# Kernel optimization log

Hardware: AMD Instinct MI355X
Metric: run time of the kernel (lower is better)

## Reference

```python
import jax, jax.numpy as jnp
import numpy as np

QMAX = 127.0

def fake_quant(x):
    # per-tensor symmetric int8 fake quantize-dequantize (QAT)
    s = jnp.maximum(jnp.max(jnp.abs(x)) / QMAX, 1e-8)
    q = jnp.clip(jnp.round(x / s), -QMAX, QMAX) * s
    return x + jax.lax.stop_gradient(q - x)  # STE

def qlinear(x, w, b):
    # x already fake-quantized by caller (input_quantizer); weights fake-quantized here
    return jnp.einsum('btc,oc->bto', x, fake_quant(w)) + b

def layer_norm(x, g, b, eps=1e-5):
    m = jnp.mean(x, axis=-1, keepdims=True)
    v = jnp.var(x, axis=-1, keepdims=True)
    return (x - m) * jax.lax.rsqrt(v + eps) * g + b

def setup_inputs() -> dict:
    key = jax.random.key(0)
    ks = jax.random.split(key, 8)
    B, T, C, I = 8, 512, 1024, 4096
    sd = 0.02
    return {
        'hidden_states': jax.random.normal(ks[0], (B, T, C), jnp.float32),
        'attention_mask': jnp.ones((B, T), jnp.float32),
        'ln1_g': jnp.ones((C,), jnp.float32), 'ln1_b': jnp.zeros((C,), jnp.float32),
        'ln2_g': jnp.ones((C,), jnp.float32), 'ln2_b': jnp.zeros((C,), jnp.float32),
        'w_qkv': sd * jax.random.normal(ks[1], (3 * C, C), jnp.float32),
        'b_qkv': jnp.zeros((3 * C,), jnp.float32),
        'w_out': sd * jax.random.normal(ks[2], (C, C), jnp.float32),
        'b_out': jnp.zeros((C,), jnp.float32),
        'w1': sd * jax.random.normal(ks[3], (I, C), jnp.float32),
        'b1': jnp.zeros((I,), jnp.float32),
        'w2': sd * jax.random.normal(ks[4], (C, I), jnp.float32),
        'b2': jnp.zeros((C,), jnp.float32),
    }

def reference(hidden_states, attention_mask, ln1_g, ln1_b, ln2_g, ln2_b,
              w_qkv, b_qkv, w_out, b_out, w1, b1, w2, b2):
    B, T, C = hidden_states.shape
    H = 16
    Dh = C // H
    scale = Dh ** -0.5

    # --- attention branch (pre-norm) ---
    x = layer_norm(hidden_states, ln1_g, ln1_b)
    qkv = qlinear(fake_quant(x), w_qkv, b_qkv)            # [B,T,3C]
    qkv = qkv.reshape(B, T, 3, H, Dh).transpose(2, 0, 3, 1, 4)
    q, k, v = qkv[0], qkv[1], qkv[2]                       # [B,H,T,Dh]
    scores = jnp.einsum('bhqd,bhkd->bhqk', q, k) * scale
    ext = (1.0 - attention_mask)[:, None, None, :] * -10000.0
    scores = scores + ext
    attn = jax.nn.softmax(scores, axis=-1)
    out = jnp.einsum('bhqk,bhkd->bhqd', attn, v)
    out = out.transpose(0, 2, 1, 3).reshape(B, T, C)
    attn_out = qlinear(fake_quant(out), w_out, b_out)
    h = hidden_states + attn_out

    # --- MLP branch (pre-norm) ---
    x = layer_norm(h, ln2_g, ln2_b)
    x = qlinear(fake_quant(x), w1, b1)
    x = jax.nn.gelu(x, approximate=False)
    x = qlinear(fake_quant(x), w2, b2)
    return h + x
```

## Files before the change

kernel.cpp:

```cpp
#include <hip/hip_runtime.h>

typedef __attribute__((ext_vector_type(8))) short bf16x8;
typedef __attribute__((ext_vector_type(4))) float f32x4;
typedef __attribute__((ext_vector_type(4))) int i32x4;
typedef unsigned short u16;
typedef unsigned int u32;

#define B_ 8
#define T_ 512
#define C_ 1024
#define I_ 4096
#define H_ 16
#define Dh_ 64
#define BT (B_*T_)
#define NH (B_*H_)

__device__ __forceinline__ float bf2f(u16 u) {
  return __uint_as_float(((u32)u) << 16);
}
__device__ __forceinline__ u16 f2bf(float f) {
  u32 u = __float_as_uint(f);
  u32 r = u + 0x7FFFu + ((u >> 16) & 1u);
  return (u16)(r >> 16);
}
__device__ __forceinline__ float wredMax(float v) {
#pragma unroll
  for (int o = 32; o; o >>= 1) v = fmaxf(v, __shfl_xor(v, o));
  return v;
}
__device__ __forceinline__ float wredSum(float v) {
#pragma unroll
  for (int o = 32; o; o >>= 1) v += __shfl_xor(v, o);
  return v;
}
__device__ __forceinline__ void slotAtomicMax(u32* arr, int bid, float bm) {
  u32 b = __float_as_uint(bm);
  volatile u32* p = arr + ((bid & 63) << 4);
  if (b > *p) atomicMax((u32*)p, b);
}
__device__ __forceinline__ float slotMax(const u32* __restrict__ arr) {
  float m = 0.f;
#pragma unroll
  for (int i = 0; i < 64; ++i) m = fmaxf(m, __uint_as_float(arr[i << 4]));
  return m;
}
__device__ __forceinline__ void gload16(const void* g, void* l) {
  __builtin_amdgcn_global_load_lds((const __attribute__((address_space(1))) void*)g,
                                   (__attribute__((address_space(3))) void*)l, 16, 0, 0);
}
__device__ __forceinline__ int qi(float v, float inv) {
  return (int)fminf(fmaxf(rintf(v * inv), -127.f), 127.f);
}
__device__ __forceinline__ float gelu1(float v) {
  float x2 = v * v;
  float e = __expf(v * fmaf(-0.0713548755f, x2, -1.5957691216f));
  return v * __builtin_amdgcn_rcpf(1.0f + e);
}

__global__ void k_init(u32* s) {
  int i = blockIdx.x * 256 + threadIdx.x;
  if (i < 8192) s[i] = 0u;
}

__global__ __launch_bounds__(256) void k_absmax4(
    const float* __restrict__ p0, int n0,
    const float* __restrict__ p1, int n1,
    const float* __restrict__ p2, int n2,
    const float* __restrict__ p3, int n3,
    u32* __restrict__ sc) {
  int stride = gridDim.x * blockDim.x;
  int gid = blockIdx.x * blockDim.x + threadIdx.x;
  float m0 = 0.f, m1 = 0.f, m2 = 0.f, m3 = 0.f;
  for (int i = gid; i < n0; i += stride) {
    float4 v = ((const float4*)p0)[i];
    m0 = fmaxf(m0, fmaxf(fmaxf(fabsf(v.x), fabsf(v.y)), fmaxf(fabsf(v.z), fabsf(v.w))));
  }
  for (int i = gid; i < n1; i += stride) {
    float4 v = ((const float4*)p1)[i];
    m1 = fmaxf(m1, fmaxf(fmaxf(fabsf(v.x), fabsf(v.y)), fmaxf(fabsf(v.z), fabsf(v.w))));
  }
  for (int i = gid; i < n2; i += stride) {
    float4 v = ((const float4*)p2)[i];
    m2 = fmaxf(m2, fmaxf(fmaxf(fabsf(v.x), fabsf(v.y)), fmaxf(fabsf(v.z), fabsf(v.w))));
  }
  for (int i = gid; i < n3; i += stride) {
    float4 v = ((const float4*)p3)[i];
    m3 = fmaxf(m3, fmaxf(fmaxf(fabsf(v.x), fabsf(v.y)), fmaxf(fabsf(v.z), fabsf(v.w))));
  }
  m0 = wredMax(m0); m1 = wredMax(m1); m2 = wredMax(m2); m3 = wredMax(m3);
  __shared__ float red[4][4];
  int wid = threadIdx.x >> 6, lane = threadIdx.x & 63;
  if (lane == 0) { red[wid][0] = m0; red[wid][1] = m1; red[wid][2] = m2; red[wid][3] = m3; }
  __syncthreads();
  if (threadIdx.x < 4) {
    int j = threadIdx.x;
    float bm = fmaxf(fmaxf(red[0][j], red[1][j]), fmaxf(red[2][j], red[3][j]));
    slotAtomicMax(sc + j * 1024, blockIdx.x, bm);
  }
}

__global__ __launch_bounds__(256) void k_quant4(
    const float* __restrict__ p0, signed char* __restrict__ q0, int n0,
    const float* __restrict__ p1, signed char* __restrict__ q1, int n1,
    const float* __restrict__ p2, signed char* __restrict__ q2, int n2,
    const float* __restrict__ p3, signed char* __restrict__ q3, int n3,
    const u32* __restrict__ sc) {
  int stride = gridDim.x * blockDim.x;
  int gid = blockIdx.x * blockDim.x + threadIdx.x;
#define QLOOP(p, q, n, slot)                                                        \
  {                                                                                 \
    float s = fmaxf(slotMax(sc + slot * 1024) * (1.0f / 127.0f), 1e-8f);            \
    float inv = 1.0f / s;                                                           \
    for (int i = gid; i < n; i += stride) {                                         \
      float4 v = ((const float4*)p)[i];                                             \
      u32 pk = (u32)(qi(v.x, inv) & 255) | ((u32)(qi(v.y, inv) & 255) << 8) |       \
               ((u32)(qi(v.z, inv) & 255) << 16) | ((u32)(qi(v.w, inv) & 255) << 24); \
      ((u32*)q)[i] = pk;                                                            \
    }                                                                               \
  }
  QLOOP(p0, q0, n0, 0)
  QLOOP(p1, q1, n1, 1)
  QLOOP(p2, q2, n2, 2)
  QLOOP(p3, q3, n3, 3)
#undef QLOOP
}

__global__ __launch_bounds__(256) void k_quant_b8(const u16* __restrict__ x, signed char* __restrict__ q,
                                                  int n8, const u32* __restrict__ arr) {
  float s = fmaxf(slotMax(arr) * (1.0f / 127.0f), 1e-8f);
  float inv = 1.0f / s;
  int stride = gridDim.x * blockDim.x;
  for (int i = blockIdx.x * blockDim.x + threadIdx.x; i < n8; i += stride) {
    uint4 d = ((const uint4*)x)[i];
    u16* e = (u16*)&d;
    uint2 o;
    o.x = (u32)(qi(bf2f(e[0]), inv) & 255) | ((u32)(qi(bf2f(e[1]), inv) & 255) << 8) |
          ((u32)(qi(bf2f(e[2]), inv) & 255) << 16) | ((u32)(qi(bf2f(e[3]), inv) & 255) << 24);
    o.y = (u32)(qi(bf2f(e[4]), inv) & 255) | ((u32)(qi(bf2f(e[5]), inv) & 255) << 8) |
          ((u32)(qi(bf2f(e[6]), inv) & 255) << 16) | ((u32)(qi(bf2f(e[7]), inv) & 255) << 24);
    ((uint2*)q)[i] = o;
  }
}

__global__ __launch_bounds__(256) void k_ln(const float* __restrict__ x, const float* __restrict__ g,
                                            const float* __restrict__ b, u16* __restrict__ y,
                                            u32* __restrict__ arr) {
  int row = blockIdx.x;
  int t = threadIdx.x;
  float4 v = ((const float4*)(x + (long)row * C_))[t];
  float s1 = v.x + v.y + v.z + v.w;
  float s2 = v.x * v.x + v.y * v.y + v.z * v.z + v.w * v.w;
  s1 = wredSum(s1);
  s2 = wredSum(s2);
  __shared__ float red[8];
  int wid = t >> 6, lane = t & 63;
  if (lane == 0) { red[wid] = s1; red[4 + wid] = s2; }
  __syncthreads();
  s1 = red[0] + red[1] + red[2] + red[3];
  s2 = red[4] + red[5] + red[6] + red[7];
  float mean = s1 * (1.0f / C_);
  float var = s2 * (1.0f / C_) - mean * mean;
  float inv = rsqrtf(var + 1e-5f);
  float4 gv = ((const float4*)g)[t];
  float4 bv = ((const float4*)b)[t];
  float4 o;
  o.x = (v.x - mean) * inv * gv.x + bv.x;
  o.y = (v.y - mean) * inv * gv.y + bv.y;
  o.z = (v.z - mean) * inv * gv.z + bv.z;
  o.w = (v.w - mean) * inv * gv.w + bv.w;
  ushort4 ob;
  ob.x = f2bf(o.x); ob.y = f2bf(o.y); ob.z = f2bf(o.z); ob.w = f2bf(o.w);
  ((ushort4*)(y + (long)row * C_))[t] = ob;
  float m = fmaxf(fmaxf(fabsf(o.x), fabsf(o.y)), fmaxf(fabsf(o.z), fabsf(o.w)));
  m = wredMax(m);
  __syncthreads();
  if (lane == 0) red[wid] = m;
  __syncthreads();
  if (t == 0) {
    float bm = fmaxf(fmaxf(red[0], red[1]), fmaxf(red[2], red[3]));
    slotAtomicMax(arr, row, bm);
  }
}

__global__ __launch_bounds__(256, 1) void k_attn(
    const u16* __restrict__ qkv, const float* __restrict__ mask,
    u16* __restrict__ O, u32* __restrict__ amax) {
  __shared__ u16 Ke[512 * 64];
  __shared__ u16 Vt[64 * 512];
  __shared__ u16 Pl[4 * 64 * 40];
  __shared__ float extl[512];
  __shared__ float redm[4];
  const int tid = threadIdx.x;
  const int w = tid >> 6, l = tid & 63;
  const int head = blockIdx.x;
  const int chunk = blockIdx.y;
  const int b = head >> 4, h = head & 15;
  const long rowbase = (long)(b * 512) * (3 * C_);

  {
    const u16* Kg = qkv + rowbase + C_ + h * 64;
    int lr8 = l >> 3;
    int ls = (l & 7) ^ lr8;
    const long koff = (long)lr8 * (3 * C_) + ls * 8;
#pragma unroll
    for (int i = 0; i < 16; ++i) {
      int r0 = w * 128 + i * 8;
      gload16(Kg + (long)r0 * (3 * C_) + koff, &Ke[r0 * 64]);
    }
  }
  {
    const u16* Vg = qkv + rowbase + 2 * C_ + h * 64;
    int kvl = tid & 31;
    int d0 = (tid >> 5) * 8;
#pragma unroll 4
    for (int i = 0; i < 16; ++i) {
      int kv = i * 32 + kvl;
      uint4 t4 = *(const uint4*)(Vg + (long)kv * (3 * C_) + d0);
      u16* tv = (u16*)&t4;
      int slot = kv >> 3, within = kv & 7;
#pragma unroll
      for (int j = 0; j < 8; ++j) {
        int d = d0 + j;
        Vt[d * 512 + ((slot ^ (d & 7)) << 3) + within] = tv[j];
      }
    }
  }
  {
    const float* mb = mask + b * 512;
    extl[tid] = (1.0f - mb[tid]) * -10000.0f;
    extl[tid + 256] = (1.0f - mb[tid + 256]) * -10000.0f;
  }
  const int qbase = chunk * 256 + w * 64;
  bf16x8 qf[4][2];
  {
    const u16* Qg = qkv + rowbase + h * 64;
#pragma unroll
    for (int qt = 0; qt < 4; ++qt)
#pragma unroll
      for (int dc = 0; dc < 2; ++dc)
        qf[qt][dc] = *(const bf16x8*)(Qg + (long)(qbase + qt * 16 + (l & 15)) * (3 * C_) + dc * 32 + (l >> 4) * 8);
  }
  __syncthreads();

  f32x4 oacc[4][4];
  float mrun[4], lrun[4];
#pragma unroll
  for (int qt = 0; qt < 4; ++qt) { mrun[qt] = -3.0e38f; lrun[qt] = 0.f; }
#pragma unroll
  for (int dt = 0; dt < 4; ++dt)
#pragma unroll
    for (int qt = 0; qt < 4; ++qt) oacc[dt][qt] = (f32x4){0.f, 0.f, 0.f, 0.f};

  u16* Pw = &Pl[w * 64 * 40];

  for (int ks = 0; ks < 16; ++ks) {
    bf16x8 kf[2][2];
#pragma unroll
    for (int kvt = 0; kvt < 2; ++kvt) {
      int kv = ks * 32 + kvt * 16 + (l & 15);
#pragma unroll
      for (int dc = 0; dc < 2; ++dc) {
        int phys = (dc * 4 + (l >> 4)) ^ (kv & 7);
        kf[kvt][dc] = *(const bf16x8*)&Ke[kv * 64 + phys * 8];
      }
    }
    f32x4 sacc[2][4];
#pragma unroll
    for (int kvt = 0; kvt < 2; ++kvt)
#pragma unroll
      for (int qt = 0; qt < 4; ++qt) {
        f32x4 a = (f32x4){0.f, 0.f, 0.f, 0.f};
        a = __builtin_amdgcn_mfma_f32_16x16x32_bf16(kf[kvt][0], qf[qt][0], a, 0, 0, 0);
        a = __builtin_amdgcn_mfma_f32_16x16x32_bf16(kf[kvt][1], qf[qt][1], a, 0, 0, 0);
        sacc[kvt][qt] = a;
      }
#pragma unroll
    for (int kvt = 0; kvt < 2; ++kvt) {
      f32x4 ev = *(const f32x4*)&extl[ks * 32 + kvt * 16 + (l >> 4) * 4];
#pragma unroll
      for (int qt = 0; qt < 4; ++qt)
#pragma unroll
        for (int r = 0; r < 4; ++r)
          sacc[kvt][qt][r] = fmaf(sacc[kvt][qt][r], 0.125f, ev[r]);
    }
#pragma unroll
    for (int qt = 0; qt < 4; ++qt) {
      float pm = sacc[0][qt][0];
#pragma unroll
      for (int r = 1; r < 4; ++r) pm = fmaxf(pm, sacc[0][qt][r]);
#pragma unroll
      for (int r = 0; r < 4; ++r) pm = fmaxf(pm, sacc[1][qt][r]);
      pm = fmaxf(pm, __shfl_xor(pm, 16));
      pm = fmaxf(pm, __shfl_xor(pm, 32));
      float mnew = fmaxf(mrun[qt], pm);
      float f = __expf(mrun[qt] - mnew);
      mrun[qt] = mnew;
      float lsum = 0.f;
#pragma unroll
      for (int kvt = 0; kvt < 2; ++kvt)
#pragma unroll
        for (int r = 0; r < 4; ++r) {
          float p = __expf(sacc[kvt][qt][r] - mnew);
          sacc[kvt][qt][r] = p;
          lsum += p;
        }
      lsum += __shfl_xor(lsum, 16);
      lsum += __shfl_xor(lsum, 32);
      lrun[qt] = lrun[qt] * f + lsum;
#pragma unroll
      for (int dt = 0; dt < 4; ++dt)
#pragma unroll
        for (int r = 0; r < 4; ++r) oacc[dt][qt][r] *= f;
#pragma unroll
      for (int kvt = 0; kvt < 2; ++kvt) {
        u32 p01 = (u32)f2bf(sacc[kvt][qt][0]) | ((u32)f2bf(sacc[kvt][qt][1]) << 16);
        u32 p23 = (u32)f2bf(sacc[kvt][qt][2]) | ((u32)f2bf(sacc[kvt][qt][3]) << 16);
        u16* pr = Pw + (qt * 16 + (l & 15)) * 40 + kvt * 16 + (l >> 4) * 4;
        *(u32*)pr = p01;
        *(u32*)(pr + 2) = p23;
      }
    }
    bf16x8 vf[4], pf[4];
#pragma unroll
    for (int dt = 0; dt < 4; ++dt) {
      int d = dt * 16 + (l & 15);
      int phys = (ks * 4 + (l >> 4)) ^ (d & 7);
      vf[dt] = *(const bf16x8*)&Vt[d * 512 + phys * 8];
    }
#pragma unroll
    for (int qt = 0; qt < 4; ++qt)
      pf[qt] = *(const bf16x8*)(Pw + (qt * 16 + (l & 15)) * 40 + (l >> 4) * 8);
#pragma unroll
    for (int dt = 0; dt < 4; ++dt)
#pragma unroll
      for (int qt = 0; qt < 4; ++qt)
        oacc[dt][qt] = __builtin_amdgcn_mfma_f32_16x16x32_bf16(vf[dt], pf[qt], oacc[dt][qt], 0, 0, 0);
  }

  float lmax = 0.f;
  u16* Ob = O + (long)(b * 512 + qbase) * C_ + h * 64;
#pragma unroll
  for (int qt = 0; qt < 4; ++qt) {
    float inv = 1.0f / lrun[qt];
    long qoff = (long)(qt * 16 + (l & 15)) * C_;
#pragma unroll
    for (int dt = 0; dt < 4; ++dt) {
      int d = dt * 16 + (l >> 4) * 4;
      float v0 = oacc[dt][qt][0] * inv;
      float v1 = oacc[dt][qt][1] * inv;
      float v2 = oacc[dt][qt][2] * inv;
      float v3 = oacc[dt][qt][3] * inv;
      lmax = fmaxf(fmaxf(lmax, fmaxf(fabsf(v0), fabsf(v1))), fmaxf(fabsf(v2), fabsf(v3)));
      u32 a01 = (u32)f2bf(v0) | ((u32)f2bf(v1) << 16);
      u32 a23 = (u32)f2bf(v2) | ((u32)f2bf(v3) << 16);
      *(u32*)(Ob + qoff + d) = a01;
      *(u32*)(Ob + qoff + d + 2) = a23;
    }
  }
  lmax = wredMax(lmax);
  if (l == 0) redm[w] = lmax;
  __syncthreads();
  if (tid == 0)
    slotAtomicMax(amax, blockIdx.x * 2 + blockIdx.y,
                  fmaxf(fmaxf(redm[0], redm[1]), fmaxf(redm[2], redm[3])));
}

template <int BM, int BN, int EPI, bool SWZ>
__global__ __launch_bounds__(256) void k_gemmq(
    const signed char* __restrict__ A, int lda,
    const signed char* __restrict__ Bm, int ldb,
    const float* __restrict__ bias,
    void* __restrict__ Cp, int ldc,
    int M, int N, int K,
    const float* __restrict__ resid,
    u32* __restrict__ amaxOut,
    const u32* __restrict__ amaxA, const u32* __restrict__ amaxB) {
  constexpr int BK = 128;
  constexpr int MF = (BM / 2) / 16;
  constexpr int NF = (BN / 2) / 16;
  constexpr int NLD = BM / 32 + BN / 32;
  __shared__ __align__(16) signed char As[2][BM * BK];
  __shared__ __align__(16) signed char Bs[2][BN * BK];
  const int tid = threadIdx.x;
  const int wid = tid >> 6, lane = tid & 63;
  const int wr = wid >> 1, wc = wid & 1;

  float sa = fmaxf(slotMax(amaxA) * (1.0f / 127.0f), 1e-8f);
  float sb = fmaxf(slotMax(amaxB) * (1.0f / 127.0f), 1e-8f);
  const float sAB = sa * sb;

  int bx = blockIdx.x, by = blockIdx.y;
  if (SWZ) {
    int gx = gridDim.x;
    int nwg = gx * gridDim.y;
    int bid = by * gx + bx;
    int cpx = nwg >> 3;
    int swz = (bid & 7) * cpx + (bid >> 3);
    bx = swz % gx;
    by = swz / gx;
  }

  const signed char* Ab = A + (long)by * BM * lda;
  const signed char* Bb = Bm + (long)bx * BN * ldb;

  i32x4 acc[MF][NF];
#pragma unroll
  for (int m = 0; m < MF; m++)
#pragma unroll
    for (int n = 0; n < NF; n++) acc[m][n] = (i32x4){0, 0, 0, 0};

  const int lr = lane & 15;
  const int l8 = lane >> 3;
  const int s8 = (lane & 7) ^ l8;
  const long aoff = (long)l8 * lda + s8 * 16;
  const long boff = (long)l8 * ldb + s8 * 16;

  auto stageAB = [&](int buf, int k0) {
#pragma unroll
    for (int i = 0; i < BM / 32; ++i) {
      int R0 = wid * (BM / 4) + i * 8;
      gload16(Ab + (long)R0 * lda + k0 + aoff, &As[buf][R0 * BK]);
    }
#pragma unroll
    for (int i = 0; i < BN / 32; ++i) {
      int R0 = wid * (BN / 4) + i * 8;
      gload16(Bb + (long)R0 * ldb + k0 + boff, &Bs[buf][R0 * BK]);
    }
  };

  auto waitCounted = [&]() {
    if constexpr (NLD == 8) {
      asm volatile("s_waitcnt vmcnt(8)" ::: "memory");
    } else if constexpr (NLD == 6) {
      asm volatile("s_waitcnt vmcnt(6)" ::: "memory");
    } else {
      asm volatile("s_waitcnt vmcnt(4)" ::: "memory");
    }
  };

  auto computeK = [&](int buf) {
#pragma unroll
    for (int kk = 0; kk < 2; ++kk) {
      const int sl = (kk << 2) + (lane >> 4);
      const int sf = (sl ^ (lr & 7)) << 4;
      i32x4 af[MF], bfr[NF];
#pragma unroll
      for (int m = 0; m < MF; m++)
        af[m] = *(const i32x4*)&As[buf][(wr * (BM / 2) + m * 16 + lr) * BK + sf];
#pragma unroll
      for (int n = 0; n < NF; n++)
        bfr[n] = *(const i32x4*)&Bs[buf][(wc * (BN / 2) + n * 16 + lr) * BK + sf];
      __builtin_amdgcn_s_setprio(1);
#pragma unroll
      for (int m = 0; m < MF; m++)
#pragma unroll
        for (int n = 0; n < NF; n++)
          acc[m][n] = __builtin_amdgcn_mfma_i32_16x16x64_i8(af[m], bfr[n], acc[m][n], 0, 0, 0);
      __builtin_amdgcn_s_setprio(0);
    }
  };

  const int nt = K / BK;
  stageAB(0, 0);
  int cur = 0;
  for (int t = 0; t < nt; ++t) {
    if (t + 1 < nt) {
      stageAB(cur ^ 1, (t + 1) * BK);
      waitCounted();
    } else {
      asm volatile("s_waitcnt vmcnt(0)" ::: "memory");
    }
    __builtin_amdgcn_s_barrier();
    computeK(cur);
    if (t + 1 < nt)
      __builtin_amdgcn_s_barrier();
    cur ^= 1;
  }

  const int rowBase = by * BM + wr * (BM / 2);
  const int colBase = bx * BN + wc * (BN / 2);
  float lmax = 0.f;
#pragma unroll
  for (int m = 0; m < MF; m++) {
    int row0 = rowBase + m * 16 + (lane >> 4) * 4;
#pragma unroll
    for (int n = 0; n < NF; n++) {
      int col = colBase + n * 16 + lr;
      float bs = bias[col];
#pragma unroll
      for (int j = 0; j < 4; j++) {
        int row = row0 + j;
        long idx = (long)row * ldc + col;
        float v = (float)acc[m][n][j] * sAB;
        if (EPI == 0) {
          ((u16*)Cp)[idx] = f2bf(v + bs);
        } else if (EPI == 1) {
          ((float*)Cp)[idx] = v + bs + resid[idx];
        } else if (EPI == 2) {
          v = gelu1(v + bs);
          lmax = fmaxf(fmaxf(lmax, v), 0.0f - v);
          ((u16*)Cp)[idx] = f2bf(v);
        } else if (EPI == 3) {
          ((float*)Cp)[idx] = v + bs + resid[idx];
        }
      }
    }
  }
  if (EPI == 2) {
    __shared__ float redm[4];
    float wm = wredMax(lmax);
    if (lane == 0) redm[wid] = wm;
    __syncthreads();
    if (tid == 0) {
      float bm = fmaxf(fmaxf(redm[0], redm[1]), fmaxf(redm[2], redm[3]));
      slotAtomicMax(amaxOut, blockIdx.y * gridDim.x + blockIdx.x, bm);
    }
  }
}

__global__ __launch_bounds__(512, 1) void k_gemmq8(
    const signed char* __restrict__ A, int lda,
    const signed char* __restrict__ Bm, int ldb,
    const float* __restrict__ bias,
    u16* __restrict__ Cp, int ldc,
    int K,
    u32* __restrict__ amaxOut,
    const u32* __restrict__ amaxA, const u32* __restrict__ amaxB) {
  __shared__ __align__(16) signed char As[2][256 * 128];
  __shared__ __align__(16) signed char Bs[2][256 * 128];
  const int tid = threadIdx.x;
  const int wid = tid >> 6, lane = tid & 63;
  const int wr = wid >> 2, wc = wid & 3;
  const int lr = lane & 15;

  float sa = fmaxf(slotMax(amaxA) * (1.0f / 127.0f), 1e-8f);
  float sb = fmaxf(slotMax(amaxB) * (1.0f / 127.0f), 1e-8f);
  const float sAB = sa * sb;

  int bx = blockIdx.x, by = blockIdx.y;
  {
    int bid = by * 16 + bx;
    int swz = (bid & 7) * 32 + (bid >> 3);
    bx = swz & 15;
    by = swz >> 4;
  }
  const signed char* Ab = A + (long)by * 256 * lda;
  const signed char* Bb = Bm + (long)bx * 256 * ldb;

  i32x4 acc[8][4];
#pragma unroll
  for (int m = 0; m < 8; m++)
#pragma unroll
    for (int n = 0; n < 4; n++) acc[m][n] = (i32x4){0, 0, 0, 0};

  const int l8 = lane >> 3;
  const int s8 = (lane & 7) ^ l8;
  const long aoff = (long)l8 * lda + s8 * 16;
  const long boff = (long)l8 * ldb + s8 * 16;

  auto stageHalf = [&](int buf, int kt, int h) {
    int k0 = kt * 128;
    if (h < 2) {
      int R0 = h * 128 + wid * 16;
      gload16(Ab + (long)R0 * lda + k0 + aoff, &As[buf][R0 * 128]);
      gload16(Ab + (long)(R0 + 8) * lda + k0 + aoff, &As[buf][(R0 + 8) * 128]);
    } else {
      int R0 = (h - 2) * 128 + wid * 16;
      gload16(Bb + (long)R0 * ldb + k0 + boff, &Bs[buf][R0 * 128]);
      gload16(Bb + (long)(R0 + 8) * ldb + k0 + boff, &Bs[buf][(R0 + 8) * 128]);
    }
  };

  const int nt = K / 128;
#define PHASE(BUF, MH, KS, STAGESTMT)                                              \
  {                                                                                \
    const int slotl = (KS) * 4 + (lane >> 4);                                      \
    i32x4 af[4], bfr[4];                                                           \
    _Pragma("unroll") for (int i = 0; i < 4; ++i) {                                \
      int row = wr * 128 + ((MH) * 4 + i) * 16 + lr;                               \
      af[i] = *(const i32x4*)&As[BUF][row * 128 + ((slotl ^ (row & 7)) << 4)];     \
    }                                                                              \
    _Pragma("unroll") for (int n = 0; n < 4; ++n) {                                \
      int row = wc * 64 + n * 16 + lr;                                             \
      bfr[n] = *(const i32x4*)&Bs[BUF][row * 128 + ((slotl ^ (row & 7)) << 4)];    \
    }                                                                              \
    STAGESTMT;                                                                     \
    __builtin_amdgcn_s_barrier();                                                  \
    __builtin_amdgcn_s_setprio(1);                                                 \
    _Pragma("unroll") for (int i = 0; i < 4; ++i)                                  \
      _Pragma("unroll") for (int n = 0; n < 4; ++n)                                \
        acc[(MH) * 4 + i][n] =                                                     \
            __builtin_amdgcn_mfma_i32_16x16x64_i8(af[i], bfr[n], acc[(MH) * 4 + i][n], 0, 0, 0); \
    __builtin_amdgcn_s_setprio(0);                                                 \
    __builtin_amdgcn_s_barrier();                                                  \
  }

  stageHalf(0, 0, 0);
  stageHalf(0, 0, 2);
  stageHalf(0, 0, 3);
  stageHalf(0, 0, 1);

  int cur = 0;
  for (int t = 0; t < nt; ++t) {
    const bool stg = (t + 1 < nt);
    const int nb = cur ^ 1;
    const int tn = t + 1;
    asm volatile("s_waitcnt vmcnt(2)" ::: "memory");
    __builtin_amdgcn_s_barrier();
    PHASE(cur, 0, 0, { if (stg) stageHalf(nb, tn, 0); })
    PHASE(cur, 0, 1, { if (stg) stageHalf(nb, tn, 2); })
    if (stg) {
      asm volatile("s_waitcnt vmcnt(4)" ::: "memory");
    } else {
      asm volatile("s_waitcnt vmcnt(0)" ::: "memory");
    }
    __builtin_amdgcn_s_barrier();
    PHASE(cur, 1, 0, { if (stg) stageHalf(nb, tn, 3); })
    PHASE(cur, 1, 1, { if (stg) stageHalf(nb, tn, 1); })
    cur = nb;
  }
#undef PHASE

  const int rowBase = by * 256 + wr * 128;
  const int colBase = bx * 256 + wc * 64;
  float lmax = 0.f;
#pragma unroll
  for (int m = 0; m < 8; m++) {
    int row0 = rowBase + m * 16 + (lane >> 4) * 4;
#pragma unroll
    for (int n = 0; n < 4; n++) {
      int col = colBase + n * 16 + lr;
      float bs = bias[col];
#pragma unroll
      for (int j = 0; j < 4; j++) {
        long idx = (long)(row0 + j) * ldc + col;
        float v = gelu1((float)acc[m][n][j] * sAB + bs);
        lmax = fmaxf(fmaxf(lmax, v), 0.0f - v);
        Cp[idx] = f2bf(v);
      }
    }
  }
  {
    __shared__ float redm[8];
    float wm = wredMax(lmax);
    if (lane == 0) redm[wid] = wm;
    __syncthreads();
    if (tid == 0) {
      float bm = redm[0];
#pragma unroll
      for (int i = 1; i < 8; ++i) bm = fmaxf(bm, redm[i]);
      slotAtomicMax(amaxOut, blockIdx.y * gridDim.x + blockIdx.x, bm);
    }
  }
}

extern "C" void kernel_launch(void* const* d_in, const int* in_sizes, int n_in,
                              void* d_out, int out_size, void* d_ws, size_t ws_size,
                              hipStream_t stream) {
  const float* hidden = (const float*)d_in[0];
  const float* mask = (const float*)d_in[1];
  const float* ln1g = (const float*)d_in[2];
  const float* ln1b = (const float*)d_in[3];
  const float* ln2g = (const float*)d_in[4];
  const float* ln2b = (const float*)d_in[5];
  const float* w_qkv = (const float*)d_in[6];
  const float* b_qkv = (const float*)d_in[7];
  const float* w_out = (const float*)d_in[8];
  const float* b_out = (const float*)d_in[9];
  const float* w1 = (const float*)d_in[10];
  const float* b1 = (const float*)d_in[11];
  const float* w2 = (const float*)d_in[12];
  const float* b2 = (const float*)d_in[13];

  char* ws = (char*)d_ws;
  u32* sc = (u32*)ws;
  const long MB = 1024 * 1024;
  signed char* wq_qkv = (signed char*)(ws + 1 * MB);
  signed char* wq_out = (signed char*)(ws + 4 * MB);
  signed char* wq_w1  = (signed char*)(ws + 6 * MB);
  signed char* wq_w2  = (signed char*)(ws + 10 * MB);
  signed char* xq     = (signed char*)(ws + 14 * MB);
  u16* x1             = (u16*)(ws + 18 * MB);
  signed char* Oq     = (signed char*)(ws + 26 * MB);
  u16* O              = (u16*)(ws + 30 * MB);
  u16* qkv            = (u16*)(ws + 38 * MB);
  float* hbuf         = (float*)(ws + 62 * MB);
  u16* y1             = (u16*)(ws + 78 * MB);
  signed char* y1q    = (signed char*)(ws + 110 * MB);

  k_init<<<32, 256, 0, stream>>>(sc);

  k_absmax4<<<512, 256, 0, stream>>>(
      w_qkv, 3 * C_ * C_ / 4, w_out, C_ * C_ / 4, w1, I_ * C_ / 4, w2, C_ * I_ / 4, sc);
  k_quant4<<<512, 256, 0, stream>>>(
      w_qkv, wq_qkv, 3 * C_ * C_ / 4, w_out, wq_out, C_ * C_ / 4,
      w1, wq_w1, I_ * C_ / 4, w2, wq_w2, C_ * I_ / 4, sc);

  k_ln<<<BT, 256, 0, stream>>>(hidden, ln1g, ln1b, x1, sc + 4 * 1024);
  k_quant_b8<<<512, 256, 0, stream>>>(x1, xq, BT * C_ / 8, sc + 4 * 1024);

  k_gemmq<128, 128, 0, true><<<dim3(24, 32), 256, 0, stream>>>(
      xq, C_, wq_qkv, C_, b_qkv, qkv, 3 * C_,
      BT, 3 * C_, C_, nullptr, nullptr, sc + 4 * 1024, sc + 0 * 1024);

  k_attn<<<dim3(NH, 2), 256, 0, stream>>>(qkv, mask, O, sc + 5 * 1024);
  k_quant_b8<<<512, 256, 0, stream>>>(O, Oq, BT * C_ / 8, sc + 5 * 1024);

  k_gemmq<64, 64, 1, true><<<dim3(16, 64), 256, 0, stream>>>(
      Oq, C_, wq_out, C_, b_out, hbuf, C_,
      BT, C_, C_, hidden, nullptr, sc + 5 * 1024, sc + 1 * 1024);

  k_ln<<<BT, 256, 0, stream>>>(hbuf, ln2g, ln2b, x1, sc + 6 * 1024);
  k_quant_b8<<<512, 256, 0, stream>>>(x1, xq, BT * C_ / 8, sc + 6 * 1024);

  k_gemmq8<<<dim3(16, 16), 512, 0, stream>>>(
      xq, C_, wq_w1, C_, b1, y1, I_, C_,
      sc + 7 * 1024, sc + 6 * 1024, sc + 2 * 1024);
  k_quant_b8<<<512, 256, 0, stream>>>(y1, y1q, BT * I_ / 8, sc + 7 * 1024);

  k_gemmq<64, 64, 3, true><<<dim3(16, 64), 256, 0, stream>>>(
      y1q, I_, wq_w2, I_, b2, d_out, C_,
      BT, C_, I_, hbuf, nullptr, sc + 7 * 1024, sc + 3 * 1024);
}
```

Baseline: 241.6 us.

## Merge weight prequant with first layernorm and store residual h in bf16

Fuses weight absmax with the first layernorm into one launch, and weight quantization with the activation quantization into a second launch. This removes two kernel launches and lets the independent work share the GPU. It also stores the intermediate residual h as bf16 instead of fp32, halving its write and its two reads (LN2 input and final residual). The cost is reduced precision in the residual path, which may move outputs away from the fp32 reference.

```diff
diff --git a/kernel.cpp b/kernel.cpp
--- a/kernel.cpp
+++ b/kernel.cpp
@@ -62,67 +62,127 @@
   if (i < 8192) s[i] = 0u;
 }
 
-__global__ __launch_bounds__(256) void k_absmax4(
+__global__ __launch_bounds__(256) void k_pre1(
     const float* __restrict__ p0, int n0,
     const float* __restrict__ p1, int n1,
     const float* __restrict__ p2, int n2,
     const float* __restrict__ p3, int n3,
-    u32* __restrict__ sc) {
-  int stride = gridDim.x * blockDim.x;
-  int gid = blockIdx.x * blockDim.x + threadIdx.x;
-  float m0 = 0.f, m1 = 0.f, m2 = 0.f, m3 = 0.f;
-  for (int i = gid; i < n0; i += stride) {
-    float4 v = ((const float4*)p0)[i];
-    m0 = fmaxf(m0, fmaxf(fmaxf(fabsf(v.x), fabsf(v.y)), fmaxf(fabsf(v.z), fabsf(v.w))));
-  }
-  for (int i = gid; i < n1; i += stride) {
-    float4 v = ((const float4*)p1)[i];
-    m1 = fmaxf(m1, fmaxf(fmaxf(fabsf(v.x), fabsf(v.y)), fmaxf(fabsf(v.z), fabsf(v.w))));
-  }
-  for (int i = gid; i < n2; i += stride) {
-    float4 v = ((const float4*)p2)[i];
-    m2 = fmaxf(m2, fmaxf(fmaxf(fabsf(v.x), fabsf(v.y)), fmaxf(fabsf(v.z), fabsf(v.w))));
-  }
-  for (int i = gid; i < n3; i += stride) {
-    float4 v = ((const float4*)p3)[i];
-    m3 = fmaxf(m3, fmaxf(fmaxf(fabsf(v.x), fabsf(v.y)), fmaxf(fabsf(v.z), fabsf(v.w))));
-  }
-  m0 = wredMax(m0); m1 = wredMax(m1); m2 = wredMax(m2); m3 = wredMax(m3);
-  __shared__ float red[4][4];
-  int wid = threadIdx.x >> 6, lane = threadIdx.x & 63;
-  if (lane == 0) { red[wid][0] = m0; red[wid][1] = m1; red[wid][2] = m2; red[wid][3] = m3; }
-  __syncthreads();
-  if (threadIdx.x < 4) {
-    int j = threadIdx.x;
-    float bm = fmaxf(fmaxf(red[0][j], red[1][j]), fmaxf(red[2][j], red[3][j]));
-    slotAtomicMax(sc + j * 1024, blockIdx.x, bm);
-  }
-}
-
-__global__ __launch_bounds__(256) void k_quant4(
+    u32* __restrict__ scw,
+    const float* __restrict__ x, const float* __restrict__ g,
+    const float* __restrict__ b, u16* __restrict__ y,
+    u32* __restrict__ arr) {
+  const int t = threadIdx.x;
+  if (blockIdx.x < 512) {
+    int stride = 512 * 256;
+    int gid = blockIdx.x * 256 + t;
+    float m0 = 0.f, m1 = 0.f, m2 = 0.f, m3 = 0.f;
+    for (int i = gid; i < n0; i += stride) {
+      float4 v = ((const float4*)p0)[i];
+      m0 = fmaxf(m0, fmaxf(fmaxf(fabsf(v.x), fabsf(v.y)), fmaxf(fabsf(v.z), fabsf(v.w))));
+    }
+    for (int i = gid; i < n1; i += stride) {
+      float4 v = ((const float4*)p1)[i];
+      m1 = fmaxf(m1, fmaxf(fmaxf(fabsf(v.x), fabsf(v.y)), fmaxf(fabsf(v.z), fabsf(v.w))));
+    }
+    for (int i = gid; i < n2; i += stride) {
+      float4 v = ((const float4*)p2)[i];
+      m2 = fmaxf(m2, fmaxf(fmaxf(fabsf(v.x), fabsf(v.y)), fmaxf(fabsf(v.z), fabsf(v.w))));
+    }
+    for (int i = gid; i < n3; i += stride) {
+      float4 v = ((const float4*)p3)[i];
+      m3 = fmaxf(m3, fmaxf(fmaxf(fabsf(v.x), fabsf(v.y)), fmaxf(fabsf(v.z), fabsf(v.w))));
+    }
+    m0 = wredMax(m0); m1 = wredMax(m1); m2 = wredMax(m2); m3 = wredMax(m3);
+    __shared__ float red4[4][4];
+    int wid = t >> 6, lane = t & 63;
+    if (lane == 0) { red4[wid][0] = m0; red4[wid][1] = m1; red4[wid][2] = m2; red4[wid][3] = m3; }
+    __syncthreads();
+    if (t < 4) {
+      int j = t;
+      float bm = fmaxf(fmaxf(red4[0][j], red4[1][j]), fmaxf(red4[2][j], red4[3][j]));
+      slotAtomicMax(scw + j * 1024, blockIdx.x, bm);
+    }
+  } else {
+    int row = blockIdx.x - 512;
+    float4 v = ((const float4*)(x + (long)row * C_))[t];
+    float s1 = v.x + v.y + v.z + v.w;
+    float s2 = v.x * v.x + v.y * v.y + v.z * v.z + v.w * v.w;
+    s1 = wredSum(s1);
+    s2 = wredSum(s2);
+    __shared__ float red[8];
+    int wid = t >> 6, lane = t & 63;
+    if (lane == 0) { red[wid] = s1; red[4 + wid] = s2; }
+    __syncthreads();
+    s1 = red[0] + red[1] + red[2] + red[3];
+    s2 = red[4] + red[5] + red[6] + red[7];
+    float mean = s1 * (1.0f / C_);
+    float var = s2 * (1.0f / C_) - mean * mean;
+    float inv = rsqrtf(var + 1e-5f);
+    float4 gv = ((const float4*)g)[t];
+    float4 bv = ((const float4*)b)[t];
+    float4 o;
+    o.x = (v.x - mean) * inv * gv.x + bv.x;
+    o.y = (v.y - mean) * inv * gv.y + bv.y;
+    o.z = (v.z - mean) * inv * gv.z + bv.z;
+    o.w = (v.w - mean) * inv * gv.w + bv.w;
+    ushort4 ob;
+    ob.x = f2bf(o.x); ob.y = f2bf(o.y); ob.z = f2bf(o.z); ob.w = f2bf(o.w);
+    ((ushort4*)(y + (long)row * C_))[t] = ob;
+    float m = fmaxf(fmaxf(fabsf(o.x), fabsf(o.y)), fmaxf(fabsf(o.z), fabsf(o.w)));
+    m = wredMax(m);
+    __syncthreads();
+    if (lane == 0) red[wid] = m;
+    __syncthreads();
+    if (t == 0) {
+      float bm = fmaxf(fmaxf(red[0], red[1]), fmaxf(red[2], red[3]));
+      slotAtomicMax(arr, row, bm);
+    }
+  }
+}
+
+__global__ __launch_bounds__(256) void k_pre2(
     const float* __restrict__ p0, signed char* __restrict__ q0, int n0,
     const float* __restrict__ p1, signed char* __restrict__ q1, int n1,
     const float* __restrict__ p2, signed char* __restrict__ q2, int n2,
     const float* __restrict__ p3, signed char* __restrict__ q3, int n3,
-    const u32* __restrict__ sc) {
-  int stride = gridDim.x * blockDim.x;
-  int gid = blockIdx.x * blockDim.x + threadIdx.x;
+    const u32* __restrict__ scw,
+    const u16* __restrict__ xb, signed char* __restrict__ xq, int n8,
+    const u32* __restrict__ arrX) {
+  const int t = threadIdx.x;
+  if (blockIdx.x < 512) {
+    int stride = 512 * 256;
+    int gid = blockIdx.x * 256 + t;
 #define QLOOP(p, q, n, slot)                                                        \
-  {                                                                                 \
-    float s = fmaxf(slotMax(sc + slot * 1024) * (1.0f / 127.0f), 1e-8f);            \
-    float inv = 1.0f / s;                                                           \
-    for (int i = gid; i < n; i += stride) {                                         \
-      float4 v = ((const float4*)p)[i];                                             \
-      u32 pk = (u32)(qi(v.x, inv) & 255) | ((u32)(qi(v.y, inv) & 255) << 8) |       \
-               ((u32)(qi(v.z, inv) & 255) << 16) | ((u32)(qi(v.w, inv) & 255) << 24); \
-      ((u32*)q)[i] = pk;                                                            \
-    }                                                                               \
-  }
-  QLOOP(p0, q0, n0, 0)
-  QLOOP(p1, q1, n1, 1)
-  QLOOP(p2, q2, n2, 2)
-  QLOOP(p3, q3, n3, 3)
+    {                                                                               \
+      float s = fmaxf(slotMax(scw + slot * 1024) * (1.0f / 127.0f), 1e-8f);         \
+      float inv = 1.0f / s;                                                         \
+      for (int i = gid; i < n; i += stride) {                                       \
+        float4 v = ((const float4*)p)[i];                                           \
+        u32 pk = (u32)(qi(v.x, inv) & 255) | ((u32)(qi(v.y, inv) & 255) << 8) |     \
+                 ((u32)(qi(v.z, inv) & 255) << 16) | ((u32)(qi(v.w, inv) & 255) << 24); \
+        ((u32*)q)[i] = pk;                                                          \
+      }                                                                             \
+    }
+    QLOOP(p0, q0, n0, 0)
+    QLOOP(p1, q1, n1, 1)
+    QLOOP(p2, q2, n2, 2)
+    QLOOP(p3, q3, n3, 3)
 #undef QLOOP
+  } else {
+    float s = fmaxf(slotMax(arrX) * (1.0f / 127.0f), 1e-8f);
+    float inv = 1.0f / s;
+    int stride = 512 * 256;
+    for (int i = (blockIdx.x - 512) * 256 + t; i < n8; i += stride) {
+      uint4 d = ((const uint4*)xb)[i];
+      u16* e = (u16*)&d;
+      uint2 o;
+      o.x = (u32)(qi(bf2f(e[0]), inv) & 255) | ((u32)(qi(bf2f(e[1]), inv) & 255) << 8) |
+            ((u32)(qi(bf2f(e[2]), inv) & 255) << 16) | ((u32)(qi(bf2f(e[3]), inv) & 255) << 24);
+      o.y = (u32)(qi(bf2f(e[4]), inv) & 255) | ((u32)(qi(bf2f(e[5]), inv) & 255) << 8) |
+            ((u32)(qi(bf2f(e[6]), inv) & 255) << 16) | ((u32)(qi(bf2f(e[7]), inv) & 255) << 24);
+      ((uint2*)xq)[i] = o;
+    }
+  }
 }
 
 __global__ __launch_bounds__(256) void k_quant_b8(const u16* __restrict__ x, signed char* __restrict__ q,
@@ -142,12 +202,14 @@
   }
 }
 
-__global__ __launch_bounds__(256) void k_ln(const float* __restrict__ x, const float* __restrict__ g,
-                                            const float* __restrict__ b, u16* __restrict__ y,
-                                            u32* __restrict__ arr) {
+__global__ __launch_bounds__(256) void k_lnb(const u16* __restrict__ x, const float* __restrict__ g,
+                                             const float* __restrict__ b, u16* __restrict__ y,
+                                             u32* __restrict__ arr) {
   int row = blockIdx.x;
   int t = threadIdx.x;
-  float4 v = ((const float4*)(x + (long)row * C_))[t];
+  ushort4 xb = ((const ushort4*)(x + (long)row * C_))[t];
+  float4 v;
+  v.x = bf2f(xb.x); v.y = bf2f(xb.y); v.z = bf2f(xb.z); v.w = bf2f(xb.w);
   float s1 = v.x + v.y + v.z + v.w;
   float s2 = v.x * v.x + v.y * v.y + v.z * v.z + v.w * v.w;
   s1 = wredSum(s1);
@@ -372,7 +434,7 @@
     const float* __restrict__ bias,
     void* __restrict__ Cp, int ldc,
     int M, int N, int K,
-    const float* __restrict__ resid,
+    const void* __restrict__ resid,
     u32* __restrict__ amaxOut,
     const u32* __restrict__ amaxA, const u32* __restrict__ amaxB) {
   constexpr int BK = 128;
@@ -495,13 +557,13 @@
         if (EPI == 0) {
           ((u16*)Cp)[idx] = f2bf(v + bs);
         } else if (EPI == 1) {
-          ((float*)Cp)[idx] = v + bs + resid[idx];
+          ((u16*)Cp)[idx] = f2bf(v + bs + ((const float*)resid)[idx]);
         } else if (EPI == 2) {
           v = gelu1(v + bs);
           lmax = fmaxf(fmaxf(lmax, v), 0.0f - v);
           ((u16*)Cp)[idx] = f2bf(v);
         } else if (EPI == 3) {
-          ((float*)Cp)[idx] = v + bs + resid[idx];
+          ((float*)Cp)[idx] = v + bs + bf2f(((const u16*)resid)[idx]);
         }
       }
     }
@@ -684,20 +746,20 @@
   signed char* Oq     = (signed char*)(ws + 26 * MB);
   u16* O              = (u16*)(ws + 30 * MB);
   u16* qkv            = (u16*)(ws + 38 * MB);
-  float* hbuf         = (float*)(ws + 62 * MB);
+  u16* hbuf           = (u16*)(ws + 62 * MB);
   u16* y1             = (u16*)(ws + 78 * MB);
   signed char* y1q    = (signed char*)(ws + 110 * MB);
 
   k_init<<<32, 256, 0, stream>>>(sc);
 
-  k_absmax4<<<512, 256, 0, stream>>>(
-      w_qkv, 3 * C_ * C_ / 4, w_out, C_ * C_ / 4, w1, I_ * C_ / 4, w2, C_ * I_ / 4, sc);
-  k_quant4<<<512, 256, 0, stream>>>(
+  k_pre1<<<512 + BT, 256, 0, stream>>>(
+      w_qkv, 3 * C_ * C_ / 4, w_out, C_ * C_ / 4, w1, I_ * C_ / 4, w2, C_ * I_ / 4, sc,
+      hidden, ln1g, ln1b, x1, sc + 4 * 1024);
+
+  k_pre2<<<1024, 256, 0, stream>>>(
       w_qkv, wq_qkv, 3 * C_ * C_ / 4, w_out, wq_out, C_ * C_ / 4,
-      w1, wq_w1, I_ * C_ / 4, w2, wq_w2, C_ * I_ / 4, sc);
-
-  k_ln<<<BT, 256, 0, stream>>>(hidden, ln1g, ln1b, x1, sc + 4 * 1024);
-  k_quant_b8<<<512, 256, 0, stream>>>(x1, xq, BT * C_ / 8, sc + 4 * 1024);
+      w1, wq_w1, I_ * C_ / 4, w2, wq_w2, C_ * I_ / 4, sc,
+      x1, xq, BT * C_ / 8, sc + 4 * 1024);
 
   k_gemmq<128, 128, 0, true><<<dim3(24, 32), 256, 0, stream>>>(
       xq, C_, wq_qkv, C_, b_qkv, qkv, 3 * C_,
@@ -710,7 +772,7 @@
       Oq, C_, wq_out, C_, b_out, hbuf, C_,
       BT, C_, C_, hidden, nullptr, sc + 5 * 1024, sc + 1 * 1024);
 
-  k_ln<<<BT, 256, 0, stream>>>(hbuf, ln2g, ln2b, x1, sc + 6 * 1024);
+  k_lnb<<<BT, 256, 0, stream>>>(hbuf, ln2g, ln2b, x1, sc + 6 * 1024);
   k_quant_b8<<<512, 256, 0, stream>>>(x1, xq, BT * C_ / 8, sc + 6 * 1024);
 
   k_gemmq8<<<dim3(16, 16), 512, 0, stream>>>(
```

Result: no change. 238.7 us, median of 2 (-1.2%).
